# Performance work log

Hardware: AMD Instinct MI355X
Metric: run time of the kernel (lower is better)

Reference implementation:

```python
import jax, jax.numpy as jnp
import numpy as np

B, T, D, H, DK = 4, 2048, 1024, 16, 64
DV = 2 * DK
QKD = H * DK           # 1024
VD = H * DV            # 2048
KW = 4                 # conv kernel size
EPS = 1e-5


def zc_rms(x, scale):
    # zero-centered RMS norm over last axis
    xc = x - jnp.mean(x, axis=-1, keepdims=True)
    return xc * jax.lax.rsqrt(jnp.mean(xc * xc, axis=-1, keepdims=True) + EPS) * scale


def causal_dwconv(x, kern, bias):
    # depthwise causal conv1d: x [B,T,C], kern [K,C], bias [C]
    k = kern.shape[0]
    t = x.shape[1]
    xp = jnp.pad(x, ((0, 0), (k - 1, 0), (0, 0)))
    out = bias
    for i in range(k):  # small fixed K=4
        out = out + xp[:, i:i + t, :] * kern[i]
    return out


def _forward(x, q_w, k_w, v_w, q_scale, k_scale, v_scale,
             q_conv_k, q_conv_b, k_conv_k, k_conv_b, v_conv_k, v_conv_b,
             alpha_w, beta_w, out_w, gate_w):
    # Q/K/V: Dense -> zero-centered RMSNorm -> causal depthwise conv -> SiLU
    q = jax.nn.silu(causal_dwconv(zc_rms(x @ q_w, q_scale), q_conv_k, q_conv_b))
    k = jax.nn.silu(causal_dwconv(zc_rms(x @ k_w, k_scale), k_conv_k, k_conv_b))
    v = jax.nn.silu(causal_dwconv(zc_rms(x @ v_w, v_scale), v_conv_k, v_conv_b))

    q = q.reshape(B, T, H, DK)
    k = k.reshape(B, T, H, DK)
    v = v.reshape(B, T, H, DV)

    alpha = jax.nn.sigmoid(x @ alpha_w)  # [B,T,H] per-head decay gate
    beta = jax.nn.sigmoid(x @ beta_w)    # [B,T,H] per-head write strength

    def step(S, inp):
        # S: [B,H,DK,DV]
        qt, kt, vt, at, bt = inp
        Sd = at[..., None, None] * S                              # gated decay
        pred = jnp.einsum('bhd,bhdv->bhv', kt, Sd)                # current memory readout at k
        S_new = Sd + bt[..., None, None] * jnp.einsum('bhd,bhv->bhdv', kt, vt - pred)  # delta rule
        ot = jnp.einsum('bhd,bhdv->bhv', qt, S_new)
        return S_new, ot

    xs = (jnp.transpose(q, (1, 0, 2, 3)),
          jnp.transpose(k, (1, 0, 2, 3)),
          jnp.transpose(v, (1, 0, 2, 3)),
          jnp.transpose(alpha, (1, 0, 2)),
          jnp.transpose(beta, (1, 0, 2)))
    S0 = jnp.zeros((B, H, DK, DV), x.dtype)
    _, o = jax.lax.scan(step, S0, xs)                             # o: [T,B,H,DV]

    core = jnp.transpose(o, (1, 0, 2, 3)).reshape(B, T, VD)
    # gated linear unit output
    return (core @ out_w) * jax.nn.sigmoid(x @ gate_w)


def setup_inputs() -> dict:
    key = jax.random.key(0)
    ks = jax.random.split(key, 12)
    g = lambda i, shape, s: jax.random.normal(ks[i], shape, dtype=jnp.float32) * s
    return {
        'x': g(0, (B, T, D), 1.0),
        'q_w': g(1, (D, QKD), 0.02), 'k_w': g(2, (D, QKD), 0.02), 'v_w': g(3, (D, VD), 0.02),
        'q_scale': jnp.ones((QKD,), jnp.float32),
        'k_scale': jnp.ones((QKD,), jnp.float32),
        'v_scale': jnp.ones((VD,), jnp.float32),
        'q_conv_k': g(4, (KW, QKD), 0.1), 'q_conv_b': jnp.zeros((QKD,), jnp.float32),
        'k_conv_k': g(5, (KW, QKD), 0.1), 'k_conv_b': jnp.zeros((QKD,), jnp.float32),
        'v_conv_k': g(6, (KW, VD), 0.1), 'v_conv_b': jnp.zeros((VD,), jnp.float32),
        'alpha_w': g(7, (D, H), 0.02), 'beta_w': g(8, (D, H), 0.02),
        'out_w': g(9, (VD, D), 0.02), 'gate_w': g(10, (D, D), 0.02),
    }


def reference(x, q_w, k_w, v_w, q_scale, k_scale, v_scale,
              q_conv_k, q_conv_b, k_conv_k, k_conv_b, v_conv_k, v_conv_b,
              alpha_w, beta_w, out_w, gate_w):
    return _forward(x, q_w, k_w, v_w, q_scale, k_scale, v_scale,
                    q_conv_k, q_conv_b, k_conv_k, k_conv_b, v_conv_k, v_conv_b,
                    alpha_w, beta_w, out_w, gate_w)
```

## Files before the change

kernel.cpp:

```cpp
#include <hip/hip_runtime.h>

#define Bc   4
#define Tc   2048
#define Dc   1024
#define Hc   16
#define DKc  64
#define DVc  128
#define QKDc 1024
#define VDc  2048
#define NPRJ 5120
#define Mc   (Bc * Tc)
#define CHUNK 64
#define NCHK (Tc / CHUNK)

typedef __bf16 bf16;
typedef __bf16 bf16x4 __attribute__((ext_vector_type(4)));
typedef __bf16 bf16x8 __attribute__((ext_vector_type(8)));
typedef float  f32x4  __attribute__((ext_vector_type(4)));

__device__ __forceinline__ float bf2f(bf16 v) { return (float)v; }
__device__ __forceinline__ bf16  f2bf(float v) { return (bf16)v; }
__device__ __forceinline__ float sigmoidf_(float x) { return 1.0f / (1.0f + __expf(-x)); }
__device__ __forceinline__ f32x4 mfma16(bf16x8 a, bf16x8 b, f32x4 c) {
    return __builtin_amdgcn_mfma_f32_16x16x32_bf16(a, b, c, 0, 0, 0);
}

__device__ __forceinline__ void glds16(const bf16* g, void* l) {
    __builtin_amdgcn_global_load_lds((const __attribute__((address_space(1))) void*)g,
                                     (__attribute__((address_space(3))) void*)l, 16, 0, 0);
}

__device__ __forceinline__ bf16* swz32x64(bf16* base, int r, int k) {
    int byte = (((r << 6) + k) << 1) ^ ((r & 7) << 4);
    return (bf16*)((char*)base + byte);
}

__global__ __launch_bounds__(256) void cast_f32_bf16(const float* __restrict__ src,
                                                     bf16* __restrict__ dst, int n4) {
    int i = blockIdx.x * 256 + threadIdx.x;
    if (i < n4) {
        float4 v = ((const float4*)src)[i];
        bf16x4 o = { f2bf(v.x), f2bf(v.y), f2bf(v.z), f2bf(v.w) };
        ((bf16x4*)dst)[i] = o;
    }
}

__global__ __launch_bounds__(256) void transpose_cast(const float* __restrict__ src,
                                                      bf16* __restrict__ dst,
                                                      int R, int C) {
    __shared__ float tile[32][33];
    int c0 = blockIdx.x * 32, r0 = blockIdx.y * 32;
    int tx = threadIdx.x, ty = threadIdx.y;
#pragma unroll
    for (int i = 0; i < 32; i += 8) {
        int r = r0 + ty + i, c = c0 + tx;
        tile[ty + i][tx] = (r < R && c < C) ? src[(size_t)r * C + c] : 0.0f;
    }
    __syncthreads();
#pragma unroll
    for (int i = 0; i < 32; i += 8) {
        int rr = c0 + ty + i, cc = r0 + tx;
        if (rr < C && cc < R) dst[(size_t)rr * R + cc] = f2bf(tile[tx][ty + i]);
    }
}

#define GP_NT 20
#define GP_MT 32
#define GP_NKT 32
__global__ __launch_bounds__(512, 2) void gemm_pipe(const bf16* __restrict__ A,
                                                    const bf16* __restrict__ Bt,
                                                    bf16* __restrict__ C) {
    __shared__ __align__(16) char lds[131072];
    const int tid = threadIdx.x;
    const int wid = tid >> 6, lane = tid & 63;
    const int lm = lane & 15, lq = lane >> 4;
    const int wm = wid >> 2, wn = wid & 3;

    const int id = blockIdx.x;
    const int nid = (id & 7) * ((GP_NT * GP_MT) / 8) + (id >> 3);
    const int tn = nid % GP_NT, tm = nid / GP_NT;
    const int n0 = tn * 256, m0 = tm * 256;

    const int r0 = tid >> 2;
    const int lsx = ((tid & 3) ^ (r0 & 3)) << 3;
    const bf16* sA0 = A  + (size_t)(m0 + r0) * Dc + lsx;
    const bf16* sA1 = sA0 + (size_t)128 * Dc;
    const bf16* sB0 = Bt + (size_t)(n0 + r0) * Dc + lsx;
    const bf16* sB1 = sB0 + (size_t)128 * Dc;

    auto stageA = [&](int kt) {
        char* d = lds + ((kt & 3) << 15) + wid * 1024;
        glds16(sA0 + kt * 32, d);
        glds16(sA1 + kt * 32, d + 8192);
    };
    auto stageB = [&](int kt) {
        char* d = lds + ((kt & 3) << 15) + 16384 + wid * 1024;
        glds16(sB0 + kt * 32, d);
        glds16(sB1 + kt * 32, d + 8192);
    };

    f32x4 acc[8][4] = {};
    const int sx = (lq ^ (lm & 3)) << 3;
    const int aoff = wm * 4096 + lm * 32 + sx;
    const int boff = wn * 2048 + lm * 32 + sx;

    stageA(0); stageB(0); stageA(1); stageB(1);
    asm volatile("s_waitcnt vmcnt(4)" ::: "memory");
    __builtin_amdgcn_s_barrier();

    for (int kt = 0; kt < GP_NKT; kt++) {
        const bf16* sA = (const bf16*)(lds + ((kt & 3) << 15));
        const bf16* sB = (const bf16*)(lds + ((kt & 3) << 15) + 16384);
        bf16x8 aF[4], bF[4], aG[4];
#pragma unroll
        for (int i = 0; i < 4; i++) aF[i] = *(const bf16x8*)&sA[aoff + i * 512];
#pragma unroll
        for (int j = 0; j < 4; j++) bF[j] = *(const bf16x8*)&sB[boff + j * 512];
        if (kt + 2 < GP_NKT) stageA(kt + 2);
        __builtin_amdgcn_s_barrier();
        asm volatile("s_waitcnt lgkmcnt(0)" ::: "memory");
        __builtin_amdgcn_sched_barrier(0);
        __builtin_amdgcn_s_setprio(1);
#pragma unroll
        for (int i = 0; i < 4; i++)
#pragma unroll
            for (int j = 0; j < 4; j++)
                acc[i][j] = mfma16(aF[i], bF[j], acc[i][j]);
        __builtin_amdgcn_s_setprio(0);
        __builtin_amdgcn_s_barrier();
#pragma unroll
        for (int i = 0; i < 4; i++) aG[i] = *(const bf16x8*)&sA[aoff + (i + 4) * 512];
        if (kt + 2 < GP_NKT) stageB(kt + 2);
        __builtin_amdgcn_s_barrier();
        asm volatile("s_waitcnt lgkmcnt(0)" ::: "memory");
        __builtin_amdgcn_sched_barrier(0);
        __builtin_amdgcn_s_setprio(1);
#pragma unroll
        for (int i = 0; i < 4; i++)
#pragma unroll
            for (int j = 0; j < 4; j++)
                acc[i + 4][j] = mfma16(aG[i], bF[j], acc[i + 4][j]);
        __builtin_amdgcn_s_setprio(0);
        if (kt + 2 < GP_NKT) asm volatile("s_waitcnt vmcnt(4)" ::: "memory");
        else                 asm volatile("s_waitcnt vmcnt(0)" ::: "memory");
        __builtin_amdgcn_s_barrier();
    }

    const int rbase = m0 + wm * 128 + lq * 4;
    const int cbase = n0 + wn * 64 + lm;
#pragma unroll
    for (int i = 0; i < 8; i++)
#pragma unroll
        for (int j = 0; j < 4; j++)
#pragma unroll
            for (int rI = 0; rI < 4; rI++)
                C[(size_t)(rbase + i * 16 + rI) * NPRJ + cbase + j * 16] =
                    f2bf(acc[i][j][rI]);
}

template <typename OutT>
__global__ __launch_bounds__(256) void gemm_bt(const bf16* __restrict__ A,
                                               const bf16* __restrict__ Bt,
                                               OutT* __restrict__ C,
                                               int M, int N, int K,
                                               const bf16* __restrict__ gate,
                                               int lda, int ldc, int ldg) {
    __shared__ bf16 As[128 * 32];
    __shared__ bf16 Bs[128 * 32];

    const int n0 = blockIdx.x * 128;
    const int m0 = blockIdx.y * 128;
    const int t = threadIdx.x;
    const int wid = t >> 6, lane = t & 63;
    const int wm = (wid & 1) * 64;
    const int wn = (wid >> 1) * 64;

    f32x4 acc[4][4] = {};

    const int srow = lane >> 2;
    const int scol = (lane & 3) * 8;
    char* AsB = (char*)As;
    char* BsB = (char*)Bs;

    for (int k0 = 0; k0 < K; k0 += 32) {
        glds16(&A[(size_t)(m0 + wid * 16 + srow) * lda + k0 + scol],       AsB + wid * 1024);
        glds16(&A[(size_t)(m0 + 64 + wid * 16 + srow) * lda + k0 + scol],  AsB + 4096 + wid * 1024);
        glds16(&Bt[(size_t)(n0 + wid * 16 + srow) * K + k0 + scol],        BsB + wid * 1024);
        glds16(&Bt[(size_t)(n0 + 64 + wid * 16 + srow) * K + k0 + scol],   BsB + 4096 + wid * 1024);
        __syncthreads();

        const int kh = (lane >> 4) * 8;
        const int lm = lane & 15;
        bf16x8 a[4], b[4];
#pragma unroll
        for (int i = 0; i < 4; i++) a[i] = *(const bf16x8*)&As[(wm + i * 16 + lm) * 32 + kh];
#pragma unroll
        for (int j = 0; j < 4; j++) b[j] = *(const bf16x8*)&Bs[(wn + j * 16 + lm) * 32 + kh];
#pragma unroll
        for (int i = 0; i < 4; i++)
#pragma unroll
            for (int j = 0; j < 4; j++)
                acc[i][j] = __builtin_amdgcn_mfma_f32_16x16x32_bf16(a[i], b[j], acc[i][j], 0, 0, 0);
        __syncthreads();
    }

    const int lm = lane & 15, lq = lane >> 4;
#pragma unroll
    for (int i = 0; i < 4; i++) {
#pragma unroll
        for (int j = 0; j < 4; j++) {
#pragma unroll
            for (int rI = 0; rI < 4; rI++) {
                int row = m0 + wm + i * 16 + lq * 4 + rI;
                int col = n0 + wn + j * 16 + lm;
                float val = acc[i][j][rI];
                if (gate) {
                    float g = bf2f(gate[(size_t)row * ldg + col]);
                    val *= sigmoidf_(g);
                }
                C[(size_t)row * ldc + col] = (OutT)val;
            }
        }
    }
}

template <int L>
__global__ __launch_bounds__(256) void zc_rms_v(bf16* __restrict__ buf,
                                                const float* __restrict__ scale,
                                                int ld) {
    constexpr int NW = L / 8 / 64;
    const int row = blockIdx.x, t = threadIdx.x;
    bf16* p = buf + (size_t)row * ld;
    bf16x8 v = *(const bf16x8*)&p[t * 8];
    float xv[8], s = 0.f, s2 = 0.f;
#pragma unroll
    for (int e = 0; e < 8; e++) { xv[e] = bf2f(v[e]); s += xv[e]; s2 += xv[e] * xv[e]; }
    __shared__ float red[2][NW];
#pragma unroll
    for (int o = 32; o > 0; o >>= 1) {
        s += __shfl_down(s, o, 64);
        s2 += __shfl_down(s2, o, 64);
    }
    if ((t & 63) == 0) { red[0][t >> 6] = s; red[1][t >> 6] = s2; }
    __syncthreads();
    s = 0.f; s2 = 0.f;
#pragma unroll
    for (int wv = 0; wv < NW; wv++) { s += red[0][wv]; s2 += red[1][wv]; }
    float mean = s / (float)L;
    float inv = rsqrtf(s2 / (float)L - mean * mean + 1e-5f);
    float4 s0 = *(const float4*)&scale[t * 8];
    float4 s1 = *(const float4*)&scale[t * 8 + 4];
    float sc[8] = { s0.x, s0.y, s0.z, s0.w, s1.x, s1.y, s1.z, s1.w };
    bf16x8 o;
#pragma unroll
    for (int e = 0; e < 8; e++) o[e] = f2bf((xv[e] - mean) * inv * sc[e]);
    *(bf16x8*)&p[t * 8] = o;
}

template <int CCH>
__global__ __launch_bounds__(256) void conv_silu_v(const bf16* __restrict__ xn,
                                                   const float* __restrict__ kern,
                                                   const float* __restrict__ bias,
                                                   bf16* __restrict__ out, int ldin) {
    const int btok = blockIdx.x;
    const int tt = btok & (Tc - 1);
    const int c8 = threadIdx.x * 8;
    float4 b0 = *(const float4*)&bias[c8], b1 = *(const float4*)&bias[c8 + 4];
    float acc[8] = { b0.x, b0.y, b0.z, b0.w, b1.x, b1.y, b1.z, b1.w };
#pragma unroll
    for (int i = 0; i < 4; i++) {
        if (tt - 3 + i >= 0) {
            bf16x8 xv = *(const bf16x8*)&xn[(size_t)(btok - 3 + i) * ldin + c8];
            float4 k0 = *(const float4*)&kern[i * CCH + c8];
            float4 k1 = *(const float4*)&kern[i * CCH + c8 + 4];
            float kk[8] = { k0.x, k0.y, k0.z, k0.w, k1.x, k1.y, k1.z, k1.w };
#pragma unroll
            for (int e = 0; e < 8; e++) acc[e] += bf2f(xv[e]) * kk[e];
        }
    }
    bf16x8 o;
#pragma unroll
    for (int e = 0; e < 8; e++) {
        float y = acc[e] * sigmoidf_(acc[e]);
        o[e] = f2bf(y);
    }
    *(bf16x8*)&out[(size_t)btok * CCH + c8] = o;
}

__global__ __launch_bounds__(256) void alphabeta_mfma(const bf16* __restrict__ x,
                                                      const float* __restrict__ aw,
                                                      const float* __restrict__ bw,
                                                      float* __restrict__ af,
                                                      float* __restrict__ bfv) {
    __shared__ bf16 whi[32][136];
    __shared__ bf16 wlo[32][136];
    const int tid = threadIdx.x, wave = tid >> 6, lane = tid & 63;
    const int lm = lane & 15, lq = lane >> 4;
    const int m0 = blockIdx.x * 128;
    f32x4 acc[2][2] = {};

    for (int k0 = 0; k0 < Dc; k0 += 128) {
        for (int idx = tid; idx < 4096; idx += 256) {
            int n = idx & 31, kk = idx >> 5;
            float v = (n < 16) ? aw[(size_t)(k0 + kk) * Hc + n]
                               : bw[(size_t)(k0 + kk) * Hc + (n - 16)];
            bf16 h = f2bf(v);
            whi[n][kk] = h;
            wlo[n][kk] = f2bf(v - bf2f(h));
        }
        __syncthreads();
#pragma unroll
        for (int ks = 0; ks < 4; ks++) {
            bf16x8 bh[2], bl[2];
#pragma unroll
            for (int j = 0; j < 2; j++) {
                bh[j] = *(const bf16x8*)&whi[j * 16 + lm][ks * 32 + lq * 8];
                bl[j] = *(const bf16x8*)&wlo[j * 16 + lm][ks * 32 + lq * 8];
            }
#pragma unroll
            for (int ii = 0; ii < 2; ii++) {
                int row = m0 + wave * 32 + ii * 16 + lm;
                bf16x8 a = *(const bf16x8*)&x[(size_t)row * Dc + k0 + ks * 32 + lq * 8];
#pragma unroll
                for (int j = 0; j < 2; j++) {
                    acc[ii][j] = mfma16(a, bh[j], acc[ii][j]);
                    acc[ii][j] = mfma16(a, bl[j], acc[ii][j]);
                }
            }
        }
        __syncthreads();
    }
#pragma unroll
    for (int ii = 0; ii < 2; ii++)
#pragma unroll
        for (int rI = 0; rI < 4; rI++) {
            int row = m0 + wave * 32 + ii * 16 + lq * 4 + rI;
            af[(size_t)row * Hc + lm]  = sigmoidf_(acc[ii][0][rI]);
            bfv[(size_t)row * Hc + lm] = sigmoidf_(acc[ii][1][rI]);
        }
}

__global__ __launch_bounds__(256) void prep(bf16* __restrict__ qf,
                                            bf16* __restrict__ kf,
                                            bf16* __restrict__ vc,
                                            const float* __restrict__ af,
                                            const float* __restrict__ bfv,
                                            bf16* __restrict__ Wb,
                                            bf16* __restrict__ Mb,
                                            float* __restrict__ gamC) {
    __shared__ __align__(16) char smem[53248];
    bf16*  Kc   = (bf16*)(smem);
    bf16*  Qc   = (bf16*)(smem + 9216);
    float* DT   = (float*)(smem + 9216);
    float* Pn   = (float*)(smem + 13568);
    float* TT   = (float*)(smem + 15744);
    float* Qn   = (float*)(smem + 9216);
    bf16*  Tb   = (bf16*)(smem + 9216);
    float* As   = (float*)(smem + 18432);
    bf16*  Vtb  = (bf16*)(smem + 18432);
    float* Ts   = (float*)(smem + 35072);
    float* lg_s = (float*)(smem + 51712);
    float* bv_s = lg_s + 64;
    float* bg_s = lg_s + 128;
    float* gm_s = lg_s + 192;
    float* kr_s = lg_s + 256;

    const int c    = blockIdx.x;
    const int bh   = blockIdx.y;
    const int b    = bh >> 4, h = bh & 15;
    const int ch   = bh * NCHK + c;
    const int tok0 = b * Tc + c * CHUNK;
    const int tid  = threadIdx.x;
    const int wave = tid >> 6, lane = tid & 63;
    const int lm = lane & 15, lq = lane >> 4, kh = lq * 8;

#pragma unroll
    for (int r = 0; r < 2; r++) {
        int idx = tid + r * 256;
        int row = idx >> 3, c8 = (idx & 7) * 8;
        *(bf16x8*)&Kc[row * 72 + c8] =
            *(const bf16x8*)&kf[(size_t)(tok0 + row) * QKDc + h * DKc + c8];
        *(bf16x8*)&Qc[row * 72 + c8] =
            *(const bf16x8*)&qf[(size_t)(tok0 + row) * QKDc + h * DKc + c8];
    }
    for (int idx = tid; idx < 64 * 65; idx += 256) Ts[idx] = 0.f;
    if (tid < 64) {
        float a  = af[(size_t)(tok0 + tid) * Hc + h];
        float bb = bfv[(size_t)(tok0 + tid) * Hc + h];
        float la = __log2f(fmaxf(a, 1e-30f));
#pragma unroll
        for (int o = 1; o < 64; o <<= 1) {
            float t = __shfl_up(la, o, 64);
            if (tid >= o) la += t;
        }
        float lgC = __shfl(la, 63, 64);
        lg_s[tid] = la;
        bv_s[tid] = bb;
        float g   = exp2f(la);
        gm_s[tid] = g;
        bg_s[tid] = bb * g;
        kr_s[tid] = exp2f(lgC - la);
        if (tid == 0) gamC[ch] = exp2f(lgC);
    }
    __syncthreads();

    {
        bf16x8 ka[2], qa[2];
#pragma unroll
        for (int s = 0; s < 2; s++) {
            ka[s] = *(const bf16x8*)&Kc[(16 * wave + lm) * 72 + s * 32 + kh];
            qa[s] = *(const bf16x8*)&Qc[(16 * wave + lm) * 72 + s * 32 + kh];
        }
#pragma unroll
        for (int jt = 0; jt < 4; jt++) {
            f32x4 kkacc = {}, qkacc = {};
#pragma unroll
            for (int s = 0; s < 2; s++) {
                bf16x8 kbf = *(const bf16x8*)&Kc[(16 * jt + lm) * 72 + s * 32 + kh];
                kkacc = mfma16(ka[s], kbf, kkacc);
                qkacc = mfma16(qa[s], kbf, qkacc);
            }
#pragma unroll
            for (int rI = 0; rI < 4; rI++) {
                int i = 16 * wave + lq * 4 + rI;
                int j = 16 * jt + lm;
                float ratio = exp2f(lg_s[i] - lg_s[j]);
                As[i * 65 + j] = (j < i) ? bv_s[i] * ratio * kkacc[rI] : 0.f;
                Mb[((size_t)ch * 64 + i) * 64 + j] =
                    (j <= i) ? f2bf(ratio * qkacc[rI]) : f2bf(0.f);
            }
        }
    }
    {
#pragma unroll
        for (int r = 0; r < 2; r++) {
            int idx = tid + r * 256;
            int row = idx >> 3, c8 = (idx & 7) * 8;
            bf16x8 v = *(const bf16x8*)&Qc[row * 72 + c8];
            float g = gm_s[row];
            bf16x8 oq;
#pragma unroll
            for (int e = 0; e < 8; e++) oq[e] = f2bf(bf2f(v[e]) * g);
            *(bf16x8*)&qf[(size_t)(tok0 + row) * QKDc + h * DKc + c8] = oq;
            bf16x8 ok;
#pragma unroll
            for (int e = 0; e < 8; e++)
                ok[e] = f2bf(kr_s[c8 + e] * bf2f(Kc[(c8 + e) * 72 + row]));
            *(bf16x8*)&kf[(size_t)(tok0 + row) * QKDc + h * DKc + c8] = ok;
        }
    }
    __syncthreads();

    if (tid < 64) {
        const int g = lane >> 4, jj = lane & 15, base = lane & 48;
        float areg[16], tcol[16];
#pragma unroll
        for (int i = 0; i < 16; i++) areg[i] = As[(16 * g + i) * 65 + 16 * g + jj];
#pragma unroll
        for (int i = 0; i < 16; i++) tcol[i] = (i == jj) ? 1.f : 0.f;
#pragma unroll
        for (int i = 1; i < 16; i++) {
            float s = 0.f;
#pragma unroll
            for (int m = 0; m < i; m++)
                s = fmaf(__shfl(areg[i], base + m, 64), tcol[m], s);
            tcol[i] = (i == jj) ? 1.f : -s;
        }
#pragma unroll
        for (int i = 0; i < 16; i++) {
            Ts[(16 * g + i) * 65 + 16 * g + jj] = tcol[i];
            DT[g * 272 + jj * 17 + i] = tcol[i];
        }
    }
    __syncthreads();

    if (wave < 2) {
        const int w = wave;
        bf16x8 ah, al, bh, bl;
#pragma unroll
        for (int e = 0; e < 8; e++) {
            int k = kh + e;
            float xa = (k < 16) ? DT[2 * w * 272 + lm * 17 + k] : 0.f;
            bf16 ha = f2bf(xa); ah[e] = ha; al[e] = f2bf(xa - bf2f(ha));
            float xb = (k < 16) ? As[(16 + 32 * w + lm) * 65 + 32 * w + k] : 0.f;
            bf16 hb = f2bf(xb); bh[e] = hb; bl[e] = f2bf(xb - bf2f(hb));
        }
        f32x4 acc = {};
        acc = mfma16(ah, bh, acc); acc = mfma16(ah, bl, acc); acc = mfma16(al, bh, acc);
#pragma unroll
        for (int rI = 0; rI < 4; rI++)
            Pn[w * 272 + (lq * 4 + rI) * 17 + lm] = -acc[rI];
    }
    __syncthreads();

    if (wave < 3) {
        bf16x8 ah, al, bh, bl;
#pragma unroll
        for (int e = 0; e < 8; e++) {
            int k = kh + e;
            float xa = 0.f, xb = 0.f;
            if (k < 16) {
                if (wave == 0)      { xa = Ts[(16 + lm) * 65 + 16 + k]; xb = Pn[lm * 17 + k]; }
                else if (wave == 1) { xa = Pn[lm * 17 + k];             xb = Ts[(16 + lm) * 65 + 16 + k]; }
                else                { xa = Ts[(48 + lm) * 65 + 48 + k]; xb = Pn[272 + lm * 17 + k]; }
            }
            bf16 ha = f2bf(xa); ah[e] = ha; al[e] = f2bf(xa - bf2f(ha));
            bf16 hb = f2bf(xb); bh[e] = hb; bl[e] = f2bf(xb - bf2f(hb));
        }
        f32x4 acc = {};
        acc = mfma16(ah, bh, acc); acc = mfma16(ah, bl, acc); acc = mfma16(al, bh, acc);
#pragma unroll
        for (int rI = 0; rI < 4; rI++) {
            int ro = lq * 4 + rI;
            if (wave == 0)      Ts[(16 + ro) * 65 + lm]      = acc[rI];
            else if (wave == 1) TT[ro * 17 + lm]             = acc[rI];
            else                Ts[(48 + ro) * 65 + 32 + lm] = acc[rI];
        }
    }
    __syncthreads();

    {
        const int a = wave >> 1, bq = wave & 1;
        bf16x8 ah, al, bh, bl;
#pragma unroll
        for (int e = 0; e < 8; e++) {
            int k = kh + e;
            float xa;
            if (a == 0) xa = (k < 16) ? DT[lm * 17 + k] : TT[lm * 17 + (k - 16)];
            else        xa = (k < 16) ? 0.f : DT[272 + lm * 17 + (k - 16)];
            bf16 ha = f2bf(xa); ah[e] = ha; al[e] = f2bf(xa - bf2f(ha));
            float xb = As[(32 + 16 * bq + lm) * 65 + k];
            bf16 hb = f2bf(xb); bh[e] = hb; bl[e] = f2bf(xb - bf2f(hb));
        }
        f32x4 acc = {};
        acc = mfma16(ah, bh, acc); acc = mfma16(ah, bl, acc); acc = mfma16(al, bh, acc);
        __syncthreads();
#pragma unroll
        for (int rI = 0; rI < 4; rI++)
            Qn[(16 * a + lq * 4 + rI) * 33 + 16 * bq + lm] = -acc[rI];
    }
    __syncthreads();

    {
        const int a = wave >> 1, bq = wave & 1;
        bf16x8 ah, al, bh, bl;
#pragma unroll
        for (int e = 0; e < 8; e++) {
            int k = kh + e;
            float xa = Ts[(32 + 16 * a + lm) * 65 + 32 + k];
            bf16 ha = f2bf(xa); ah[e] = ha; al[e] = f2bf(xa - bf2f(ha));
            float xb = Qn[(16 * bq + lm) * 33 + k];
            bf16 hb = f2bf(xb); bh[e] = hb; bl[e] = f2bf(xb - bf2f(hb));
        }
        f32x4 acc = {};
        acc = mfma16(ah, bh, acc); acc = mfma16(ah, bl, acc); acc = mfma16(al, bh, acc);
#pragma unroll
        for (int rI = 0; rI < 4; rI++)
            Ts[(32 + 16 * a + lq * 4 + rI) * 65 + 16 * bq + lm] = acc[rI];
    }
    __syncthreads();

    for (int idx = tid; idx < 4096; idx += 256) {
        int i = idx >> 6, j = idx & 63;
        Tb[i * 72 + j] = f2bf(Ts[i * 65 + j]);
    }
    __syncthreads();
#pragma unroll
    for (int r = 0; r < 4; r++) {
        int idx = tid + r * 256;
        int j = idx >> 4, c8 = (idx & 15) * 8;
        bf16x8 v = *(const bf16x8*)&vc[(size_t)(tok0 + j) * VDc + h * DVc + c8];
        float bb = bv_s[j];
#pragma unroll
        for (int e = 0; e < 8; e++)
            Vtb[(c8 + e) * 72 + j] = f2bf(bf2f(v[e]) * bb);
    }
    __syncthreads();
    {
        bf16x8 ta[2];
#pragma unroll
        for (int s = 0; s < 2; s++)
            ta[s] = *(const bf16x8*)&Tb[(16 * wave + lm) * 72 + s * 32 + kh];
#pragma unroll
        for (int dt = 0; dt < 4; dt++) {
            f32x4 wacc = {};
#pragma unroll
            for (int s = 0; s < 2; s++) {
                bf16x8 wbf;
                int d = 16 * dt + lm;
#pragma unroll
                for (int e = 0; e < 8; e++) {
                    int j = s * 32 + kh + e;
                    wbf[e] = f2bf(bg_s[j] * bf2f(Kc[j * 72 + d]));
                }
                wacc = mfma16(ta[s], wbf, wacc);
            }
#pragma unroll
            for (int rI = 0; rI < 4; rI++) {
                int i = 16 * wave + lq * 4 + rI;
                Wb[((size_t)ch * 64 + i) * 64 + 16 * dt + lm] = f2bf(wacc[rI]);
            }
        }
#pragma unroll
        for (int dt = 0; dt < 8; dt++) {
            f32x4 uacc = {};
#pragma unroll
            for (int s = 0; s < 2; s++) {
                bf16x8 vb = *(const bf16x8*)&Vtb[(16 * dt + lm) * 72 + s * 32 + kh];
                uacc = mfma16(ta[s], vb, uacc);
            }
#pragma unroll
            for (int rI = 0; rI < 4; rI++) {
                int i = 16 * wave + lq * 4 + rI;
                vc[(size_t)(tok0 + i) * VDc + h * DVc + 16 * dt + lm] = f2bf(uacc[rI]);
            }
        }
    }
}

__global__ __launch_bounds__(256) void chunkloop(const bf16* __restrict__ qf,
                                                 const bf16* __restrict__ kf,
                                                 const bf16* __restrict__ vc,
                                                 const bf16* __restrict__ Wb,
                                                 const bf16* __restrict__ Mb,
                                                 const float* __restrict__ gamC,
                                                 bf16* __restrict__ o, int ldo) {
    const int vg = blockIdx.x;
    const int bh = blockIdx.y;
    const int b = bh >> 4, h = bh & 15;
    const int tid = threadIdx.x;
    const int wave = tid >> 6, lane = tid & 63;
    const int lm = lane & 15, lq = lane >> 4, kh = lq * 8;

    __shared__ __align__(16) bf16 SbBuf[32 * 64];
    __shared__ __align__(16) bf16 UtBuf[32 * 64];

    for (int idx = tid; idx < 32 * 64; idx += 256) SbBuf[idx] = f2bf(0.f);

    f32x4 Sacc[2] = {};

    const int colK = h * DKc;
    const int colV = h * DVc + vg * 32;

    bf16x8 wa[2], qa[2], ma[2], kb[2];
    bf16 uvv[2][4];

    auto loadFrags = [&](int c, bf16x8 (&wa_)[2], bf16x8 (&qa_)[2], bf16x8 (&ma_)[2],
                         bf16x8 (&kb_)[2], bf16 (&uvv_)[2][4]) {
        const int tok0 = b * Tc + c * CHUNK;
        const size_t chb = ((size_t)bh * NCHK + c) * 64;
#pragma unroll
        for (int s = 0; s < 2; s++) {
            wa_[s] = *(const bf16x8*)&Wb[(chb + 16 * wave + lm) * 64 + s * 32 + kh];
            ma_[s] = *(const bf16x8*)&Mb[(chb + 16 * wave + lm) * 64 + s * 32 + kh];
            qa_[s] = *(const bf16x8*)&qf[(size_t)(tok0 + 16 * wave + lm) * QKDc + colK + s * 32 + kh];
            kb_[s] = *(const bf16x8*)&kf[(size_t)(tok0 + 16 * wave + lm) * QKDc + colK + s * 32 + kh];
        }
#pragma unroll
        for (int dt = 0; dt < 2; dt++)
#pragma unroll
            for (int rI = 0; rI < 4; rI++)
                uvv_[dt][rI] =
                    vc[(size_t)(tok0 + 16 * wave + lq * 4 + rI) * VDc + colV + 16 * dt + lm];
    };

    loadFrags(0, wa, qa, ma, kb, uvv);
    __syncthreads();

    for (int c = 0; c < NCHK; c++) {
        const float gC = gamC[(size_t)bh * NCHK + c];
        bf16x8 sf[2][2];
#pragma unroll
        for (int dt = 0; dt < 2; dt++)
#pragma unroll
            for (int s = 0; s < 2; s++)
                sf[dt][s] = *(const bf16x8*)swz32x64(SbBuf, 16 * dt + lm, s * 32 + kh);
        f32x4 pacc[2] = {};
#pragma unroll
        for (int dt = 0; dt < 2; dt++)
#pragma unroll
            for (int s = 0; s < 2; s++)
                pacc[dt] = mfma16(wa[s], sf[dt][s], pacc[dt]);

        bf16x8 wa2[2], qa2[2], ma2[2], kb2[2];
        bf16 uvv2[2][4];
        if (c + 1 < NCHK) loadFrags(c + 1, wa2, qa2, ma2, kb2, uvv2);

#pragma unroll
        for (int dt = 0; dt < 2; dt++)
#pragma unroll
            for (int rI = 0; rI < 4; rI++) {
                float u = bf2f(uvv[dt][rI]) - pacc[dt][rI];
                *swz32x64(UtBuf, 16 * dt + lm, 16 * wave + lq * 4 + rI) = f2bf(u);
            }
        __syncthreads();

        bf16x8 uf[2][2];
#pragma unroll
        for (int dt = 0; dt < 2; dt++)
#pragma unroll
            for (int s = 0; s < 2; s++)
                uf[dt][s] = *(const bf16x8*)swz32x64(UtBuf, 16 * dt + lm, s * 32 + kh);

        f32x4 oacc[2] = {};
#pragma unroll
        for (int dt = 0; dt < 2; dt++)
#pragma unroll
            for (int s = 0; s < 2; s++) {
                oacc[dt] = mfma16(qa[s], sf[dt][s], oacc[dt]);
                oacc[dt] = mfma16(ma[s], uf[dt][s], oacc[dt]);
            }
        {
            const int tok0 = b * Tc + c * CHUNK;
#pragma unroll
            for (int dt = 0; dt < 2; dt++)
#pragma unroll
                for (int rI = 0; rI < 4; rI++)
                    o[(size_t)(tok0 + 16 * wave + lq * 4 + rI) * ldo + colV + 16 * dt + lm] =
                        f2bf(oacc[dt][rI]);
        }
#pragma unroll
        for (int dt = 0; dt < 2; dt++) {
#pragma unroll
            for (int e = 0; e < 4; e++) Sacc[dt][e] *= gC;
#pragma unroll
            for (int s = 0; s < 2; s++)
                Sacc[dt] = mfma16(uf[dt][s], kb[s], Sacc[dt]);
        }
        __syncthreads();
#pragma unroll
        for (int dt = 0; dt < 2; dt++)
#pragma unroll
            for (int rI = 0; rI < 4; rI++)
                *swz32x64(SbBuf, 16 * dt + lq * 4 + rI, 16 * wave + lm) = f2bf(Sacc[dt][rI]);
        __syncthreads();

        if (c + 1 < NCHK) {
#pragma unroll
            for (int s = 0; s < 2; s++) { wa[s] = wa2[s]; qa[s] = qa2[s]; ma[s] = ma2[s]; kb[s] = kb2[s]; }
#pragma unroll
            for (int dt = 0; dt < 2; dt++)
#pragma unroll
                for (int rI = 0; rI < 4; rI++) uvv[dt][rI] = uvv2[dt][rI];
        }
    }
}

extern "C" void kernel_launch(void* const* d_in, const int* in_sizes, int n_in,
                              void* d_out, int out_size, void* d_ws, size_t ws_size,
                              hipStream_t stream) {
    const float* x        = (const float*)d_in[0];
    const float* q_w      = (const float*)d_in[1];
    const float* k_w      = (const float*)d_in[2];
    const float* v_w      = (const float*)d_in[3];
    const float* q_scale  = (const float*)d_in[4];
    const float* k_scale  = (const float*)d_in[5];
    const float* v_scale  = (const float*)d_in[6];
    const float* q_conv_k = (const float*)d_in[7];
    const float* q_conv_b = (const float*)d_in[8];
    const float* k_conv_k = (const float*)d_in[9];
    const float* k_conv_b = (const float*)d_in[10];
    const float* v_conv_k = (const float*)d_in[11];
    const float* v_conv_b = (const float*)d_in[12];
    const float* alpha_w  = (const float*)d_in[13];
    const float* beta_w   = (const float*)d_in[14];
    const float* out_w    = (const float*)d_in[15];
    const float* gate_w   = (const float*)d_in[16];

    char* w = (char*)d_ws;
    bf16* xb  = (bf16*)w; w += (size_t)Mc * Dc * 2;
    bf16* qwT = (bf16*)w; w += (size_t)QKDc * Dc * 2;
    bf16* kwT = (bf16*)w; w += (size_t)QKDc * Dc * 2;
    bf16* vwT = (bf16*)w; w += (size_t)VDc * Dc * 2;
    bf16* gwT = (bf16*)w; w += (size_t)Dc * Dc * 2;
    bf16* owT = (bf16*)w; w += (size_t)Dc * VDc * 2;
    bf16* lin_all = (bf16*)w; w += (size_t)Mc * NPRJ * 2;
    bf16* qf = (bf16*)w; w += (size_t)Mc * QKDc * 2;
    bf16* kf = (bf16*)w; w += (size_t)Mc * QKDc * 2;
    bf16* vc = (bf16*)w; w += (size_t)Mc * VDc * 2;
    float* af = (float*)w; w += (size_t)Mc * Hc * 4;
    float* bfv = (float*)w; w += (size_t)Mc * Hc * 4;
    const int NCH_TOT = Bc * Hc * NCHK;
    bf16* Wb = (bf16*)w; w += (size_t)NCH_TOT * 64 * 64 * 2;
    bf16* Mb = (bf16*)w; w += (size_t)NCH_TOT * 64 * 64 * 2;
    float* gamC = (float*)w; w += (size_t)NCH_TOT * 4;
    bf16* o_core = lin_all;

    dim3 tb(32, 8);
    cast_f32_bf16<<<(Mc * Dc / 4 + 255) / 256, 256, 0, stream>>>(x, xb, Mc * Dc / 4);
    transpose_cast<<<dim3(QKDc / 32, Dc / 32), tb, 0, stream>>>(q_w, qwT, Dc, QKDc);
    transpose_cast<<<dim3(QKDc / 32, Dc / 32), tb, 0, stream>>>(k_w, kwT, Dc, QKDc);
    transpose_cast<<<dim3(VDc / 32, Dc / 32), tb, 0, stream>>>(v_w, vwT, Dc, VDc);
    transpose_cast<<<dim3(Dc / 32, Dc / 32), tb, 0, stream>>>(gate_w, gwT, Dc, Dc);
    transpose_cast<<<dim3(Dc / 32, VDc / 32), tb, 0, stream>>>(out_w, owT, VDc, Dc);

    gemm_pipe<<<GP_NT * GP_MT, 512, 0, stream>>>(xb, qwT, lin_all);

    zc_rms_v<QKDc><<<Mc, QKDc / 8, 0, stream>>>(lin_all,        q_scale, NPRJ);
    zc_rms_v<QKDc><<<Mc, QKDc / 8, 0, stream>>>(lin_all + 1024, k_scale, NPRJ);
    zc_rms_v<VDc><<<Mc, VDc / 8, 0, stream>>>(lin_all + 2048,   v_scale, NPRJ);

    conv_silu_v<QKDc><<<Mc, QKDc / 8, 0, stream>>>(lin_all,        q_conv_k, q_conv_b, qf, NPRJ);
    conv_silu_v<QKDc><<<Mc, QKDc / 8, 0, stream>>>(lin_all + 1024, k_conv_k, k_conv_b, kf, NPRJ);
    conv_silu_v<VDc><<<Mc, VDc / 8, 0, stream>>>(lin_all + 2048,   v_conv_k, v_conv_b, vc, NPRJ);

    alphabeta_mfma<<<Mc / 128, 256, 0, stream>>>(xb, alpha_w, beta_w, af, bfv);

    prep<<<dim3(NCHK, Bc * Hc), 256, 0, stream>>>(qf, kf, vc, af, bfv, Wb, Mb, gamC);
    chunkloop<<<dim3(4, Bc * Hc), 256, 0, stream>>>(qf, kf, vc, Wb, Mb, gamC, o_core, NPRJ);

    gemm_bt<float><<<dim3(Dc / 128, Mc / 128), 256, 0, stream>>>(
        o_core, owT, (float*)d_out, Mc, Dc, VDc, lin_all + 4096, NPRJ, Dc, NPRJ);
}
```

Before: 562.6 us.

## Deepen projection GEMM prefetch and replace output GEMM with pipelined kernel

```diff
diff --git a/kernel.cpp b/kernel.cpp
--- a/kernel.cpp
+++ b/kernel.cpp
@@ -104,9 +104,9 @@
     const int aoff = wm * 4096 + lm * 32 + sx;
     const int boff = wn * 2048 + lm * 32 + sx;
 
-    stageA(0); stageB(0); stageA(1); stageB(1);
-    asm volatile("s_waitcnt vmcnt(4)" ::: "memory");
-    __builtin_amdgcn_s_barrier();
+    stageA(0); stageB(0); stageA(1); stageB(1); stageA(2); stageB(2);
+    asm volatile("s_waitcnt vmcnt(8)" ::: "memory");
+    asm volatile("s_barrier" ::: "memory");
 
     for (int kt = 0; kt < GP_NKT; kt++) {
         const bf16* sA = (const bf16*)(lds + ((kt & 3) << 15));
@@ -116,34 +116,25 @@
         for (int i = 0; i < 4; i++) aF[i] = *(const bf16x8*)&sA[aoff + i * 512];
 #pragma unroll
         for (int j = 0; j < 4; j++) bF[j] = *(const bf16x8*)&sB[boff + j * 512];
-        if (kt + 2 < GP_NKT) stageA(kt + 2);
-        __builtin_amdgcn_s_barrier();
-        asm volatile("s_waitcnt lgkmcnt(0)" ::: "memory");
-        __builtin_amdgcn_sched_barrier(0);
+#pragma unroll
+        for (int i = 0; i < 4; i++) aG[i] = *(const bf16x8*)&sA[aoff + (i + 4) * 512];
+        if (kt + 3 < GP_NKT) { stageA(kt + 3); stageB(kt + 3); }
         __builtin_amdgcn_s_setprio(1);
 #pragma unroll
         for (int i = 0; i < 4; i++)
 #pragma unroll
             for (int j = 0; j < 4; j++)
                 acc[i][j] = mfma16(aF[i], bF[j], acc[i][j]);
-        __builtin_amdgcn_s_setprio(0);
-        __builtin_amdgcn_s_barrier();
-#pragma unroll
-        for (int i = 0; i < 4; i++) aG[i] = *(const bf16x8*)&sA[aoff + (i + 4) * 512];
-        if (kt + 2 < GP_NKT) stageB(kt + 2);
-        __builtin_amdgcn_s_barrier();
-        asm volatile("s_waitcnt lgkmcnt(0)" ::: "memory");
-        __builtin_amdgcn_sched_barrier(0);
-        __builtin_amdgcn_s_setprio(1);
 #pragma unroll
         for (int i = 0; i < 4; i++)
 #pragma unroll
             for (int j = 0; j < 4; j++)
                 acc[i + 4][j] = mfma16(aG[i], bF[j], acc[i + 4][j]);
         __builtin_amdgcn_s_setprio(0);
-        if (kt + 2 < GP_NKT) asm volatile("s_waitcnt vmcnt(4)" ::: "memory");
-        else                 asm volatile("s_waitcnt vmcnt(0)" ::: "memory");
-        __builtin_amdgcn_s_barrier();
+        if (kt + 3 < GP_NKT)      asm volatile("s_waitcnt vmcnt(8)" ::: "memory");
+        else if (kt + 2 < GP_NKT) asm volatile("s_waitcnt vmcnt(4)" ::: "memory");
+        else                      asm volatile("s_waitcnt vmcnt(0)" ::: "memory");
+        asm volatile("s_barrier" ::: "memory");
     }
 
     const int rbase = m0 + wm * 128 + lq * 4;
@@ -158,70 +149,81 @@
                     f2bf(acc[i][j][rI]);
 }
 
-template <typename OutT>
-__global__ __launch_bounds__(256) void gemm_bt(const bf16* __restrict__ A,
-                                               const bf16* __restrict__ Bt,
-                                               OutT* __restrict__ C,
-                                               int M, int N, int K,
-                                               const bf16* __restrict__ gate,
-                                               int lda, int ldc, int ldg) {
-    __shared__ bf16 As[128 * 32];
-    __shared__ bf16 Bs[128 * 32];
-
-    const int n0 = blockIdx.x * 128;
-    const int m0 = blockIdx.y * 128;
-    const int t = threadIdx.x;
-    const int wid = t >> 6, lane = t & 63;
-    const int wm = (wid & 1) * 64;
-    const int wn = (wid >> 1) * 64;
+#define GO_NKT 64
+__global__ __launch_bounds__(512, 2) void gemm_pipe_out(const bf16* __restrict__ A,
+                                                        const bf16* __restrict__ Bt,
+                                                        float* __restrict__ C,
+                                                        const bf16* __restrict__ gate) {
+    __shared__ __align__(16) char lds[98304];
+    const int tid = threadIdx.x;
+    const int wid = tid >> 6, lane = tid & 63;
+    const int lm = lane & 15, lq = lane >> 4;
+    const int wm = wid >> 2, wn = wid & 3;
+
+    const int id = blockIdx.x;
+    const int nid = (id & 7) * 32 + (id >> 3);
+    const int tm = nid >> 2, tn = nid & 3;
+    const int m0 = tm * 128, n0 = tn * 256;
+
+    const int r0 = tid >> 2;
+    const int lsx = ((tid & 3) ^ (r0 & 3)) << 3;
+    const bf16* sAp = A  + (size_t)(m0 + r0) * NPRJ + lsx;
+    const bf16* sB0 = Bt + (size_t)(n0 + r0) * VDc + lsx;
+    const bf16* sB1 = sB0 + (size_t)128 * VDc;
+
+    auto stageA = [&](int kt) {
+        glds16(sAp + kt * 32, lds + (kt & 3) * 24576 + wid * 1024);
+    };
+    auto stageB = [&](int kt) {
+        char* d = lds + (kt & 3) * 24576 + 8192 + wid * 1024;
+        glds16(sB0 + kt * 32, d);
+        glds16(sB1 + kt * 32, d + 8192);
+    };
 
     f32x4 acc[4][4] = {};
-
-    const int srow = lane >> 2;
-    const int scol = (lane & 3) * 8;
-    char* AsB = (char*)As;
-    char* BsB = (char*)Bs;
-
-    for (int k0 = 0; k0 < K; k0 += 32) {
-        glds16(&A[(size_t)(m0 + wid * 16 + srow) * lda + k0 + scol],       AsB + wid * 1024);
-        glds16(&A[(size_t)(m0 + 64 + wid * 16 + srow) * lda + k0 + scol],  AsB + 4096 + wid * 1024);
-        glds16(&Bt[(size_t)(n0 + wid * 16 + srow) * K + k0 + scol],        BsB + wid * 1024);
-        glds16(&Bt[(size_t)(n0 + 64 + wid * 16 + srow) * K + k0 + scol],   BsB + 4096 + wid * 1024);
-        __syncthreads();
-
-        const int kh = (lane >> 4) * 8;
-        const int lm = lane & 15;
+    const int sx = (lq ^ (lm & 3)) << 3;
+    const int aoff = wm * 2048 + lm * 32 + sx;
+    const int boff = wn * 2048 + lm * 32 + sx;
+
+    stageA(0); stageB(0); stageA(1); stageB(1); stageA(2); stageB(2);
+    asm volatile("s_waitcnt vmcnt(6)" ::: "memory");
+    asm volatile("s_barrier" ::: "memory");
+
+    for (int kt = 0; kt < GO_NKT; kt++) {
+        const bf16* sA = (const bf16*)(lds + (kt & 3) * 24576);
+        const bf16* sB = sA + 4096;
         bf16x8 a[4], b[4];
 #pragma unroll
-        for (int i = 0; i < 4; i++) a[i] = *(const bf16x8*)&As[(wm + i * 16 + lm) * 32 + kh];
-#pragma unroll
-        for (int j = 0; j < 4; j++) b[j] = *(const bf16x8*)&Bs[(wn + j * 16 + lm) * 32 + kh];
+        for (int i = 0; i < 4; i++) a[i] = *(const bf16x8*)&sA[aoff + i * 512];
+#pragma unroll
+        for (int j = 0; j < 4; j++) b[j] = *(const bf16x8*)&sB[boff + j * 512];
+        if (kt + 3 < GO_NKT) { stageA(kt + 3); stageB(kt + 3); }
+        __builtin_amdgcn_s_setprio(1);
 #pragma unroll
         for (int i = 0; i < 4; i++)
 #pragma unroll
             for (int j = 0; j < 4; j++)
-                acc[i][j] = __builtin_amdgcn_mfma_f32_16x16x32_bf16(a[i], b[j], acc[i][j], 0, 0, 0);
-        __syncthreads();
-    }
-
-    const int lm = lane & 15, lq = lane >> 4;
-#pragma unroll
-    for (int i = 0; i < 4; i++) {
-#pragma unroll
-        for (int j = 0; j < 4; j++) {
+                acc[i][j] = mfma16(a[i], b[j], acc[i][j]);
+        __builtin_amdgcn_s_setprio(0);
+        if (kt + 3 < GO_NKT)      asm volatile("s_waitcnt vmcnt(6)" ::: "memory");
+        else if (kt + 2 < GO_NKT) asm volatile("s_waitcnt vmcnt(3)" ::: "memory");
+        else                      asm volatile("s_waitcnt vmcnt(0)" ::: "memory");
+        asm volatile("s_barrier" ::: "memory");
+    }
+
+    const int rbase = m0 + wm * 64 + lq * 4;
+    const int cbase = n0 + wn * 64 + lm;
+#pragma unroll
+    for (int i = 0; i < 4; i++)
+#pragma unroll
+        for (int j = 0; j < 4; j++)
 #pragma unroll
             for (int rI = 0; rI < 4; rI++) {
-                int row = m0 + wm + i * 16 + lq * 4 + rI;
-                int col = n0 + wn + j * 16 + lm;
-                float val = acc[i][j][rI];
-                if (gate) {
-                    float g = bf2f(gate[(size_t)row * ldg + col]);
-                    val *= sigmoidf_(g);
-                }
-                C[(size_t)row * ldc + col] = (OutT)val;
-            }
-        }
-    }
+                int row = rbase + i * 16 + rI;
+                int col = cbase + j * 16;
+                float g = bf2f(gate[(size_t)row * NPRJ + col]);
+                C[(size_t)row * Dc + col] = acc[i][j][rI] * sigmoidf_(g);
+            }
 }
 
 template <int L>
@@ -809,6 +811,5 @@
     prep<<<dim3(NCHK, Bc * Hc), 256, 0, stream>>>(qf, kf, vc, af, bfv, Wb, Mb, gamC);
     chunkloop<<<dim3(4, Bc * Hc), 256, 0, stream>>>(qf, kf, vc, Wb, Mb, gamC, o_core, NPRJ);
 
-    gemm_bt<float><<<dim3(Dc / 128, Mc / 128), 256, 0, stream>>>(
-        o_core, owT, (float*)d_out, Mc, Dc, VDc, lin_all + 4096, NPRJ, Dc, NPRJ);
-}
+    gemm_pipe_out<<<256, 512, 0, stream>>>(o_core, owT, (float*)d_out, lin_all + 4096);
+}
```

Result: faster. 524.5 us (-6.8%).
